# Kernel optimization log

Measured on AMD Instinct MI355X. Metric: run time of the kernel, lower is better.

## Reference

```python
import jax, jax.numpy as jnp
import numpy as np

N_NODES = 100000
N_EDGES = 800000
ANNOT = 92
HID = 64
N_STEPS = 8
N_IDX = 20000


def setup_inputs() -> dict:
    key = jax.random.key(0)
    ks = jax.random.split(key, 12)
    s = 1.0 / np.sqrt(HID)
    return {
        'x': jax.random.normal(ks[0], (N_NODES, ANNOT), dtype=jnp.float32),
        'edge_index': jax.random.randint(ks[1], (2, N_EDGES), 0, N_NODES, dtype=jnp.int64),
        'idx': jax.random.randint(ks[2], (N_IDX,), 0, N_NODES, dtype=jnp.int64),
        'W_red': jax.random.normal(ks[3], (ANNOT, HID), dtype=jnp.float32) / np.sqrt(ANNOT),
        'b_red': jnp.zeros((HID,), dtype=jnp.float32),
        'W_g': jax.random.normal(ks[4], (N_STEPS, HID, HID), dtype=jnp.float32) * s,
        'w_ih': jax.random.normal(ks[5], (3 * HID, HID), dtype=jnp.float32) * s,
        'w_hh': jax.random.normal(ks[6], (3 * HID, HID), dtype=jnp.float32) * s,
        'b_ih': jax.random.normal(ks[7], (3 * HID,), dtype=jnp.float32) * s,
        'b_hh': jax.random.normal(ks[8], (3 * HID,), dtype=jnp.float32) * s,
        'W_lin': jax.random.normal(ks[9], (HID, 1), dtype=jnp.float32) * s,
        'b_lin': jnp.zeros((1,), dtype=jnp.float32),
    }


def _gru_cell(a, h, w_ih, w_hh, b_ih, b_hh):
    # a: aggregated messages [N, H]; h: hidden state [N, H]
    gi = a @ w_ih.T + b_ih  # [N, 3H]
    gh = h @ w_hh.T + b_hh
    i_r, i_z, i_n = jnp.split(gi, 3, axis=-1)
    h_r, h_z, h_n = jnp.split(gh, 3, axis=-1)
    r = jax.nn.sigmoid(i_r + h_r)
    z = jax.nn.sigmoid(i_z + h_z)
    n = jnp.tanh(i_n + r * h_n)
    return (1.0 - z) * n + z * h


def reference(x, edge_index, idx, W_red, b_red, W_g, w_ih, w_hh, b_ih, b_hh, W_lin, b_lin):
    src, dst = edge_index[0], edge_index[1]
    h = x @ W_red + b_red  # [N, H]

    def step(h, Wt):
        m = h @ Wt                                  # [N, H] per-step transform
        msg = jnp.take(m, src, axis=0)              # gather along edges [E, H]
        aggr = jax.ops.segment_sum(msg, dst, num_segments=N_NODES)  # scatter-add
        h_new = _gru_cell(aggr, h, w_ih, w_hh, b_ih, b_hh)
        return h_new, None

    h, _ = jax.lax.scan(step, h, W_g)
    sel = jnp.take(h, idx, axis=0)                  # index_select [B, H]
    return jax.nn.sigmoid(sel @ W_lin + b_lin)      # [B, 1]
```

## Files before the change

kernel.cpp:

```cpp
#include <hip/hip_runtime.h>
#include <hip/hip_bf16.h>

#define NN 100000
#define HH 64
#define AN 92
#define NSTEP 8
#define NGRP 6250
#define NB 391
#define RB 768

typedef float f4v __attribute__((ext_vector_type(4)));
typedef short s8v __attribute__((ext_vector_type(8)));

__device__ __forceinline__ float sigf(float x) { return 1.0f / (1.0f + __expf(-x)); }
__device__ __forceinline__ float tanhfast(float x) { return 1.0f - 2.0f / (1.0f + __expf(2.0f * x)); }

__device__ __forceinline__ unsigned short tobf(float x) {
    __hip_bfloat16 b = __float2bfloat16(x);
    return __builtin_bit_cast(unsigned short, b);
}
__device__ __forceinline__ float frombf(unsigned short u) {
    return __int_as_float(((unsigned)u) << 16);
}

__device__ __forceinline__ int packpos(int k, int r) {
    int T = r >> 4, kh = k >> 5;
    int lane = ((k >> 3) & 3) * 16 + (r & 15);
    int j = k & 7;
    return ((T * 2 + kh) * 64 + lane) * 8 + j;
}

__global__ __launch_bounds__(256) void k_histwcp(const int* __restrict__ dst,
                                                 int* __restrict__ cur, int E, int HB,
                                                 const float* __restrict__ Wg,
                                                 const float* __restrict__ w_ih,
                                                 const float* __restrict__ w_hh,
                                                 unsigned short* __restrict__ Wcp,
                                                 unsigned short* __restrict__ Whp) {
    __shared__ float wl[192 * 65];
    if (blockIdx.x < HB) {
        int e = blockIdx.x * 256 + threadIdx.x;
        if (e < E) atomicAdd(cur + dst[e], 1);
        return;
    }
    int wb = blockIdx.x - HB;
    if (wb < 384) {
        for (int i = threadIdx.x; i < 192 * 64; i += 256) {
            int r = i >> 6, q = i & 63;
            wl[r * 65 + q] = w_ih[i];
        }
        __syncthreads();
        int gid = wb * 256 + threadIdx.x;
        int r = gid % 192;
        int k = (gid / 192) & 63;
        int t = gid / (192 * 64);
        const float* wg = Wg + t * 4096 + k * 64;
        float acc = 0.f;
#pragma unroll
        for (int q = 0; q < 64; ++q) acc = fmaf(wg[q], wl[r * 65 + q], acc);
        Wcp[t * 12288 + packpos(k, r)] = tobf(acc);
    } else {
        int gid = (wb - 384) * 256 + threadIdx.x;
        if (gid >= 192 * 64) return;
        int r = gid >> 6, k = gid & 63;
        Whp[packpos(k, r)] = tobf(w_hh[r * 64 + k]);
    }
}

__global__ __launch_bounds__(256) void k_scan1(const int* __restrict__ cur, int* __restrict__ bsum) {
    __shared__ int ws[4];
    int gid = blockIdx.x * 256 + threadIdx.x;
    int lane = threadIdx.x & 63, wave = threadIdx.x >> 6;
    int v = (gid < NN) ? cur[gid] : 0;
#pragma unroll
    for (int off = 32; off > 0; off >>= 1) v += __shfl_xor(v, off, 64);
    if (lane == 0) ws[wave] = v;
    __syncthreads();
    if (threadIdx.x == 0) bsum[blockIdx.x] = ws[0] + ws[1] + ws[2] + ws[3];
}

__global__ __launch_bounds__(256) void k_scan3(int* __restrict__ cur, const int* __restrict__ bsum) {
    __shared__ int ws[4];
    __shared__ int ws2[4];
    int tid = threadIdx.x;
    int lane = tid & 63, wave = tid >> 6;
    int s = 0;
    for (int i = tid; i < blockIdx.x; i += 256) s += bsum[i];
#pragma unroll
    for (int off = 32; off > 0; off >>= 1) s += __shfl_xor(s, off, 64);
    if (lane == 0) ws2[wave] = s;
    int gid = blockIdx.x * 256 + tid;
    int orig = (gid < NN) ? cur[gid] : 0;
    int v = orig;
#pragma unroll
    for (int off = 1; off < 64; off <<= 1) {
        int w = __shfl_up(v, off, 64);
        if (lane >= off) v += w;
    }
    if (lane == 63) ws[wave] = v;
    __syncthreads();
    int base = ws2[0] + ws2[1] + ws2[2] + ws2[3];
    int woff = 0;
    for (int w = 0; w < 4; ++w) woff += (w < wave) ? ws[w] : 0;
    if (gid < NN) cur[gid] = v - orig + woff + base;
}

__global__ __launch_bounds__(256) void k_plred(const int* __restrict__ src,
                                               const int* __restrict__ dst,
                                               int* __restrict__ cur,
                                               int* __restrict__ srt, int E,
                                               const float* __restrict__ x,
                                               const float* __restrict__ W,
                                               const float* __restrict__ b,
                                               float* __restrict__ h,
                                               unsigned short* __restrict__ hb) {
    __shared__ float xl[16][96];
    __shared__ float wl[96 * 64];
    int tid = threadIdx.x;
    if (blockIdx.x >= RB) {
        int e = (blockIdx.x - RB) * 256 + tid;
        if (e < E) {
            int pos = atomicAdd(cur + dst[e], 1);
            srt[pos] = src[e];
        }
        return;
    }
    for (int i = tid; i < AN * 64; i += 256) wl[i] = W[i];
    wl[AN * 64 + tid] = 0.f;
    if (tid < 64) xl[tid >> 2][AN + (tid & 3)] = 0.f;
    int lane = tid & 63, wave = tid >> 6;
    float bj = b[lane];

    for (int g = blockIdx.x; g < NGRP; g += RB) {
        int n0 = g * 16;
        __syncthreads();
        for (int i = tid; i < 16 * AN; i += 256)
            xl[i / AN][i % AN] = x[(size_t)n0 * AN + i];
        __syncthreads();
        float a[4];
#pragma unroll
        for (int u = 0; u < 4; ++u) a[u] = bj;
#pragma unroll
        for (int k4 = 0; k4 < 96; k4 += 4) {
            float4 xv[4];
#pragma unroll
            for (int u = 0; u < 4; ++u) xv[u] = *(const float4*)&xl[wave * 4 + u][k4];
#pragma unroll
            for (int kk = 0; kk < 4; ++kk) {
                float wv = wl[(k4 + kk) * 64 + lane];
                a[0] = fmaf(((const float*)&xv[0])[kk], wv, a[0]);
                a[1] = fmaf(((const float*)&xv[1])[kk], wv, a[1]);
                a[2] = fmaf(((const float*)&xv[2])[kk], wv, a[2]);
                a[3] = fmaf(((const float*)&xv[3])[kk], wv, a[3]);
            }
        }
#pragma unroll
        for (int u = 0; u < 4; ++u) {
            int n = n0 + wave * 4 + u;
            h[(size_t)n * HH + lane] = a[u];
            hb[(size_t)n * HH + lane] = tobf(a[u]);
        }
    }
}

__global__ __launch_bounds__(256) void k_aggr(const unsigned short* __restrict__ hb,
                                              const int* __restrict__ cur,
                                              const int* __restrict__ srt,
                                              unsigned short* __restrict__ Sb) {
    int gid = blockIdx.x * 256 + threadIdx.x;
    int wid = gid >> 6;
    int lane = threadIdx.x & 63;
    int half = lane >> 5;
    int ci = lane & 31;
    int n = wid * 2 + half;
    if (n >= NN) return;
    int st = (n == 0) ? 0 : cur[n - 1];
    int en = cur[n];
    float aa[8], bb[8];
#pragma unroll
    for (int i = 0; i < 8; ++i) { aa[i] = 0.f; bb[i] = 0.f; }
    for (int j = st; j < en; j += 8) {
        unsigned u[8];
#pragma unroll
        for (int i = 0; i < 8; ++i) {
            int jj = j + i;
            int sidx = srt[min(jj, en - 1)];
            unsigned uu = *(const unsigned*)(hb + (size_t)sidx * HH + ci * 2);
            u[i] = (jj < en) ? uu : 0u;
        }
#pragma unroll
        for (int i = 0; i < 8; ++i) {
            aa[i] += frombf((unsigned short)u[i]);
            bb[i] += frombf((unsigned short)(u[i] >> 16));
        }
    }
    float A = ((aa[0] + aa[1]) + (aa[2] + aa[3])) + ((aa[4] + aa[5]) + (aa[6] + aa[7]));
    float B = ((bb[0] + bb[1]) + (bb[2] + bb[3])) + ((bb[4] + bb[5]) + (bb[6] + bb[7]));
    unsigned o = (unsigned)tobf(A) | ((unsigned)tobf(B) << 16);
    *(unsigned*)(Sb + (size_t)n * HH + ci * 2) = o;
}

__device__ __forceinline__ s8v cvt8(const float* __restrict__ p) {
    s8v r;
#pragma unroll
    for (int i = 0; i < 8; ++i) r[i] = (short)tobf(p[i]);
    return r;
}

__global__ __launch_bounds__(256) void k_gru(const unsigned short* __restrict__ Sb,
                                             float* __restrict__ h,
                                             unsigned short* __restrict__ hb,
                                             const unsigned short* __restrict__ Wcp_t,
                                             const unsigned short* __restrict__ Whp,
                                             const float* __restrict__ b_ih,
                                             const float* __restrict__ b_hh) {
    const s8v* wiB = (const s8v*)Wcp_t;
    const s8v* whB = (const s8v*)Whp;

    int lane = threadIdx.x & 63;
    int wave = threadIdx.x >> 6;
    int quad = lane >> 4, nidx = lane & 15;
    int g = blockIdx.x * 4 + wave;
    if (g >= NGRP) return;

    float brz[4], bzz[4], bin[4], bhn[4];
#pragma unroll
    for (int t = 0; t < 4; ++t) {
        int c = t * 16 + nidx;
        brz[t] = b_ih[c] + b_hh[c];
        bzz[t] = b_ih[64 + c] + b_hh[64 + c];
        bin[t] = b_ih[128 + c];
        bhn[t] = b_hh[128 + c];
    }

    int n0 = g * 16;
    size_t rowoff = (size_t)(n0 + nidx) * HH + quad * 8;
    s8v aS0 = *(const s8v*)(Sb + rowoff);
    s8v aS1 = *(const s8v*)(Sb + rowoff + 32);
    s8v aH0 = cvt8(h + rowoff);
    s8v aH1 = cvt8(h + rowoff + 32);

#pragma unroll
    for (int t = 0; t < 4; ++t) {
        f4v aRZ0 = {brz[t], brz[t], brz[t], brz[t]};
        f4v aRZ1 = {bzz[t], bzz[t], bzz[t], bzz[t]};
        f4v aIN  = {bin[t], bin[t], bin[t], bin[t]};
        f4v aHN  = {bhn[t], bhn[t], bhn[t], bhn[t]};
        aRZ0 = __builtin_amdgcn_mfma_f32_16x16x32_bf16(aS0, wiB[(t * 2 + 0) * 64 + lane], aRZ0, 0, 0, 0);
        aRZ0 = __builtin_amdgcn_mfma_f32_16x16x32_bf16(aS1, wiB[(t * 2 + 1) * 64 + lane], aRZ0, 0, 0, 0);
        aRZ0 = __builtin_amdgcn_mfma_f32_16x16x32_bf16(aH0, whB[(t * 2 + 0) * 64 + lane], aRZ0, 0, 0, 0);
        aRZ0 = __builtin_amdgcn_mfma_f32_16x16x32_bf16(aH1, whB[(t * 2 + 1) * 64 + lane], aRZ0, 0, 0, 0);
        int tz = t + 4;
        aRZ1 = __builtin_amdgcn_mfma_f32_16x16x32_bf16(aS0, wiB[(tz * 2 + 0) * 64 + lane], aRZ1, 0, 0, 0);
        aRZ1 = __builtin_amdgcn_mfma_f32_16x16x32_bf16(aS1, wiB[(tz * 2 + 1) * 64 + lane], aRZ1, 0, 0, 0);
        aRZ1 = __builtin_amdgcn_mfma_f32_16x16x32_bf16(aH0, whB[(tz * 2 + 0) * 64 + lane], aRZ1, 0, 0, 0);
        aRZ1 = __builtin_amdgcn_mfma_f32_16x16x32_bf16(aH1, whB[(tz * 2 + 1) * 64 + lane], aRZ1, 0, 0, 0);
        int tn = t + 8;
        aIN = __builtin_amdgcn_mfma_f32_16x16x32_bf16(aS0, wiB[(tn * 2 + 0) * 64 + lane], aIN, 0, 0, 0);
        aIN = __builtin_amdgcn_mfma_f32_16x16x32_bf16(aS1, wiB[(tn * 2 + 1) * 64 + lane], aIN, 0, 0, 0);
        aHN = __builtin_amdgcn_mfma_f32_16x16x32_bf16(aH0, whB[(tn * 2 + 0) * 64 + lane], aHN, 0, 0, 0);
        aHN = __builtin_amdgcn_mfma_f32_16x16x32_bf16(aH1, whB[(tn * 2 + 1) * 64 + lane], aHN, 0, 0, 0);
        int c = t * 16 + nidx;
#pragma unroll
        for (int reg = 0; reg < 4; ++reg) {
            int node = n0 + quad * 4 + reg;
            float rv = sigf(aRZ0[reg]);
            float zv = sigf(aRZ1[reg]);
            float nv = tanhfast(fmaf(rv, aHN[reg], aIN[reg]));
            size_t off = (size_t)node * HH + c;
            float ho = h[off];
            float hnew = fmaf(zv, ho - nv, nv);
            h[off] = hnew;
            hb[off] = tobf(hnew);
        }
    }
}

__global__ __launch_bounds__(256) void k_readout(const float* __restrict__ h,
                                                 const int* __restrict__ idx,
                                                 const float* __restrict__ Wl,
                                                 const float* __restrict__ bl,
                                                 float* __restrict__ out, int B) {
    int gid = blockIdx.x * 256 + threadIdx.x;
    int i = gid >> 6, lane = gid & 63;
    if (i >= B) return;
    int n = idx[i];
    float v = h[(size_t)n * HH + lane] * Wl[lane];
#pragma unroll
    for (int off = 32; off > 0; off >>= 1) v += __shfl_xor(v, off, 64);
    if (lane == 0) out[i] = sigf(v + bl[0]);
}

extern "C" void kernel_launch(void* const* d_in, const int* in_sizes, int n_in,
                              void* d_out, int out_size, void* d_ws, size_t ws_size,
                              hipStream_t stream) {
    const float* x     = (const float*)d_in[0];
    const int*   ei    = (const int*)d_in[1];
    const int*   idx   = (const int*)d_in[2];
    const float* W_red = (const float*)d_in[3];
    const float* b_red = (const float*)d_in[4];
    const float* W_g   = (const float*)d_in[5];
    const float* w_ih  = (const float*)d_in[6];
    const float* w_hh  = (const float*)d_in[7];
    const float* b_ih  = (const float*)d_in[8];
    const float* b_hh  = (const float*)d_in[9];
    const float* W_lin = (const float*)d_in[10];
    const float* b_lin = (const float*)d_in[11];
    float* out = (float*)d_out;
    const int E = in_sizes[1] / 2;
    const int B = in_sizes[2];
    const int* src = ei;
    const int* dst = ei + E;
    const int PB = (E + 255) / 256;

    float*          h   = (float*)d_ws;
    unsigned short* hb  = (unsigned short*)(h + (size_t)NN * HH);
    unsigned short* Sb  = hb + (size_t)NN * HH;
    unsigned short* Wcp = Sb + (size_t)NN * HH;
    unsigned short* Whp = Wcp + (size_t)NSTEP * 12288;
    int*            cur = (int*)(Whp + 12288);
    int*            srt = cur + NN;
    int*            bsum = srt + E;

    hipMemsetAsync(cur, 0, NN * sizeof(int), stream);
    k_histwcp<<<PB + 384 + 48, 256, 0, stream>>>(dst, cur, E, PB,
                                                 W_g, w_ih, w_hh, Wcp, Whp);

    k_scan1<<<NB, 256, 0, stream>>>(cur, bsum);
    k_scan3<<<NB, 256, 0, stream>>>(cur, bsum);

    k_plred<<<RB + PB, 256, 0, stream>>>(src, dst, cur, srt, E,
                                         x, W_red, b_red, h, hb);

    for (int t = 0; t < NSTEP; ++t) {
        k_aggr<<<(NN / 2 * 64 + 255) / 256, 256, 0, stream>>>(hb, cur, srt, Sb);
        k_gru<<<1563, 256, 0, stream>>>(Sb, h, hb, Wcp + (size_t)t * 12288, Whp,
                                        b_ih, b_hh);
    }

    k_readout<<<(B * 64 + 255) / 256, 256, 0, stream>>>(h, idx, W_lin, b_lin, out, B);
}
```

Measured before the change: 580.8 us.

## Chunk bf16 hidden state by feature groups and aggregate one chunk per block

Stores the bf16 hidden state and the aggregate buffer as 8 column-chunks of 8 features each, laid out [chunk][node][8], so one gathered row is a single 16-byte load. Aggregation now runs one thread per node per chunk, with blockIdx selecting the chunk. The CSR offsets and the source indices for a block are staged in shared memory, with a global-memory fallback when a block's edge span exceeds the staging buffer. The intent is a gather table per chunk that is small enough to stay cache-resident and fewer, wider loads. The trade-off is that the sorted index list is read once per chunk and the GRU kernel now writes hb with scattered 2-byte stores.

```diff
diff --git a/kernel.cpp b/kernel.cpp
--- a/kernel.cpp
+++ b/kernel.cpp
@@ -8,6 +8,7 @@
 #define NGRP 6250
 #define NB 391
 #define RB 768
+#define SPMAX 4608
 
 typedef float f4v __attribute__((ext_vector_type(4)));
 typedef short s8v __attribute__((ext_vector_type(8)));
@@ -22,6 +23,7 @@
 __device__ __forceinline__ float frombf(unsigned short u) {
     return __int_as_float(((unsigned)u) << 16);
 }
+
 
 __device__ __forceinline__ int packpos(int k, int r) {
     int T = r >> 4, kh = k >> 5;
@@ -158,46 +160,75 @@
         for (int u = 0; u < 4; ++u) {
             int n = n0 + wave * 4 + u;
             h[(size_t)n * HH + lane] = a[u];
-            hb[(size_t)n * HH + lane] = tobf(a[u]);
-        }
-    }
-}
+            hb[((size_t)(lane >> 3) * NN + n) * 8 + (lane & 7)] = tobf(a[u]);
+        }
+    }
+}
+
+#define AGGR_BODY(GETSRC)                                                     \
+    for (int j = st; j < en; j += 4) {                                        \
+        unsigned u[4][4];                                                     \
+        _Pragma("unroll")                                                     \
+        for (int i = 0; i < 4; ++i) {                                         \
+            int jj = min(j + i, en - 1);                                      \
+            int sidx = GETSRC;                                                \
+            const uint4 uu = *(const uint4*)(tab + (size_t)sidx * 8);         \
+            unsigned m = (j + i < en) ? 0xffffffffu : 0u;                     \
+            u[i][0] = uu.x & m; u[i][1] = uu.y & m;                           \
+            u[i][2] = uu.z & m; u[i][3] = uu.w & m;                           \
+        }                                                                     \
+        _Pragma("unroll")                                                     \
+        for (int i = 0; i < 4; ++i) {                                         \
+            _Pragma("unroll")                                                 \
+            for (int k = 0; k < 4; ++k) {                                     \
+                unsigned w = u[i][k];                                         \
+                acc[2 * k]     += frombf((unsigned short)w);                  \
+                acc[2 * k + 1] += frombf((unsigned short)(w >> 16));          \
+            }                                                                 \
+        }                                                                     \
+    }
 
 __global__ __launch_bounds__(256) void k_aggr(const unsigned short* __restrict__ hb,
                                               const int* __restrict__ cur,
                                               const int* __restrict__ srt,
                                               unsigned short* __restrict__ Sb) {
-    int gid = blockIdx.x * 256 + threadIdx.x;
-    int wid = gid >> 6;
-    int lane = threadIdx.x & 63;
-    int half = lane >> 5;
-    int ci = lane & 31;
-    int n = wid * 2 + half;
+    __shared__ int s_srt[SPMAX];
+    __shared__ int s_cur[257];
+    const int cg = blockIdx.x & 7;
+    const int nb = blockIdx.x >> 3;
+    const int n0 = nb * 256;
+    const int tid = threadIdx.x;
+    for (int i = tid; i < 257; i += 256) {
+        int n = n0 + i - 1;
+        s_cur[i] = (n < 0) ? 0 : cur[min(n, NN - 1)];
+    }
+    __syncthreads();
+    const int base = s_cur[0];
+    const int span = s_cur[256] - base;
+    const int sp = min(span, SPMAX);
+    for (int i = tid; i < sp; i += 256) s_srt[i] = srt[base + i];
+    __syncthreads();
+    const int n = n0 + tid;
     if (n >= NN) return;
-    int st = (n == 0) ? 0 : cur[n - 1];
-    int en = cur[n];
-    float aa[8], bb[8];
-#pragma unroll
-    for (int i = 0; i < 8; ++i) { aa[i] = 0.f; bb[i] = 0.f; }
-    for (int j = st; j < en; j += 8) {
-        unsigned u[8];
-#pragma unroll
-        for (int i = 0; i < 8; ++i) {
-            int jj = j + i;
-            int sidx = srt[min(jj, en - 1)];
-            unsigned uu = *(const unsigned*)(hb + (size_t)sidx * HH + ci * 2);
-            u[i] = (jj < en) ? uu : 0u;
-        }
-#pragma unroll
-        for (int i = 0; i < 8; ++i) {
-            aa[i] += frombf((unsigned short)u[i]);
-            bb[i] += frombf((unsigned short)(u[i] >> 16));
-        }
-    }
-    float A = ((aa[0] + aa[1]) + (aa[2] + aa[3])) + ((aa[4] + aa[5]) + (aa[6] + aa[7]));
-    float B = ((bb[0] + bb[1]) + (bb[2] + bb[3])) + ((bb[4] + bb[5]) + (bb[6] + bb[7]));
-    unsigned o = (unsigned)tobf(A) | ((unsigned)tobf(B) << 16);
-    *(unsigned*)(Sb + (size_t)n * HH + ci * 2) = o;
+    const int st = s_cur[tid];
+    const int en = s_cur[tid + 1];
+    const unsigned short* tab = hb + (size_t)cg * (NN * 8);
+    float acc[8];
+#pragma unroll
+    for (int i = 0; i < 8; ++i) acc[i] = 0.f;
+
+    if (span <= SPMAX) {
+        AGGR_BODY(s_srt[jj - base])
+    } else {
+        AGGR_BODY(srt[jj])
+    }
+
+    unsigned o0 = (unsigned)tobf(acc[0]) | ((unsigned)tobf(acc[1]) << 16);
+    unsigned o1 = (unsigned)tobf(acc[2]) | ((unsigned)tobf(acc[3]) << 16);
+    unsigned o2 = (unsigned)tobf(acc[4]) | ((unsigned)tobf(acc[5]) << 16);
+    unsigned o3 = (unsigned)tobf(acc[6]) | ((unsigned)tobf(acc[7]) << 16);
+    uint4 ov; ov.x = o0; ov.y = o1; ov.z = o2; ov.w = o3;
+    *(uint4*)(Sb + ((size_t)cg * NN + n) * 8) = ov;
 }
 
 __device__ __forceinline__ s8v cvt8(const float* __restrict__ p) {
@@ -235,8 +266,9 @@
 
     int n0 = g * 16;
     size_t rowoff = (size_t)(n0 + nidx) * HH + quad * 8;
-    s8v aS0 = *(const s8v*)(Sb + rowoff);
-    s8v aS1 = *(const s8v*)(Sb + rowoff + 32);
+    size_t soff   = ((size_t)quad * NN + (n0 + nidx)) * 8;
+    s8v aS0 = *(const s8v*)(Sb + soff);
+    s8v aS1 = *(const s8v*)(Sb + soff + (size_t)4 * NN * 8);
     s8v aH0 = cvt8(h + rowoff);
     s8v aH1 = cvt8(h + rowoff + 32);
 
@@ -261,6 +293,8 @@
         aHN = __builtin_amdgcn_mfma_f32_16x16x32_bf16(aH0, whB[(tn * 2 + 0) * 64 + lane], aHN, 0, 0, 0);
         aHN = __builtin_amdgcn_mfma_f32_16x16x32_bf16(aH1, whB[(tn * 2 + 1) * 64 + lane], aHN, 0, 0, 0);
         int c = t * 16 + nidx;
+        int chunk = c >> 3;
+        int cc = c & 7;
 #pragma unroll
         for (int reg = 0; reg < 4; ++reg) {
             int node = n0 + quad * 4 + reg;
@@ -271,7 +305,7 @@
             float ho = h[off];
             float hnew = fmaf(zv, ho - nv, nv);
             h[off] = hnew;
-            hb[off] = tobf(hnew);
+            hb[((size_t)chunk * NN + node) * 8 + cc] = tobf(hnew);
         }
     }
 }
@@ -332,8 +366,9 @@
     k_plred<<<RB + PB, 256, 0, stream>>>(src, dst, cur, srt, E,
                                          x, W_red, b_red, h, hb);
 
+    const int AGB = ((NN + 255) / 256) * 8;
     for (int t = 0; t < NSTEP; ++t) {
-        k_aggr<<<(NN / 2 * 64 + 255) / 256, 256, 0, stream>>>(hb, cur, srt, Sb);
+        k_aggr<<<AGB, 256, 0, stream>>>(hb, cur, srt, Sb);
         k_gru<<<1563, 256, 0, stream>>>(Sb, h, hb, Wcp + (size_t)t * 12288, Whp,
                                         b_ih, b_hh);
     }
```

Result: slower. 699.1 us (+20.4%).

## Fuse edge aggregation and GRU update into one per-step kernel with ping-pong bf16 state

Applied to the files above, without the earlier changes.

Merges the gather/segment-sum kernel and the MFMA GRU kernel into a single per-step kernel. Each wave first aggregates its 16 nodes into a swizzled LDS tile, then feeds the tile straight into the MFMA GRU. This removes the global round trip of the aggregate buffer and halves the launches per step. To avoid read/write races on the bf16 hidden state across nodes, it double-buffers hb between steps. The trade-off is less parallelism during aggregation: one wave now handles 8 node pairs sequentially instead of one pair, which lowers memory-level parallelism for the latency-bound gathers.

```diff
diff --git a/kernel.cpp b/kernel.cpp
--- a/kernel.cpp
+++ b/kernel.cpp
@@ -163,65 +163,70 @@
     }
 }
 
-__global__ __launch_bounds__(256) void k_aggr(const unsigned short* __restrict__ hb,
+__device__ __forceinline__ s8v cvt8(const float* __restrict__ p) {
+    s8v r;
+#pragma unroll
+    for (int i = 0; i < 8; ++i) r[i] = (short)tobf(p[i]);
+    return r;
+}
+
+__global__ __launch_bounds__(256) void k_step(const unsigned short* __restrict__ hbo,
+                                              float* __restrict__ h,
+                                              unsigned short* __restrict__ hbn,
                                               const int* __restrict__ cur,
                                               const int* __restrict__ srt,
-                                              unsigned short* __restrict__ Sb) {
-    int gid = blockIdx.x * 256 + threadIdx.x;
-    int wid = gid >> 6;
+                                              const unsigned short* __restrict__ Wcp_t,
+                                              const unsigned short* __restrict__ Whp,
+                                              const float* __restrict__ b_ih,
+                                              const float* __restrict__ b_hh) {
+    __shared__ __align__(16) unsigned char sA[4][2048];
+
     int lane = threadIdx.x & 63;
-    int half = lane >> 5;
-    int ci = lane & 31;
-    int n = wid * 2 + half;
-    if (n >= NN) return;
-    int st = (n == 0) ? 0 : cur[n - 1];
-    int en = cur[n];
-    float aa[8], bb[8];
-#pragma unroll
-    for (int i = 0; i < 8; ++i) { aa[i] = 0.f; bb[i] = 0.f; }
-    for (int j = st; j < en; j += 8) {
-        unsigned u[8];
-#pragma unroll
-        for (int i = 0; i < 8; ++i) {
-            int jj = j + i;
-            int sidx = srt[min(jj, en - 1)];
-            unsigned uu = *(const unsigned*)(hb + (size_t)sidx * HH + ci * 2);
-            u[i] = (jj < en) ? uu : 0u;
-        }
-#pragma unroll
-        for (int i = 0; i < 8; ++i) {
-            aa[i] += frombf((unsigned short)u[i]);
-            bb[i] += frombf((unsigned short)(u[i] >> 16));
-        }
-    }
-    float A = ((aa[0] + aa[1]) + (aa[2] + aa[3])) + ((aa[4] + aa[5]) + (aa[6] + aa[7]));
-    float B = ((bb[0] + bb[1]) + (bb[2] + bb[3])) + ((bb[4] + bb[5]) + (bb[6] + bb[7]));
-    unsigned o = (unsigned)tobf(A) | ((unsigned)tobf(B) << 16);
-    *(unsigned*)(Sb + (size_t)n * HH + ci * 2) = o;
-}
-
-__device__ __forceinline__ s8v cvt8(const float* __restrict__ p) {
-    s8v r;
-#pragma unroll
-    for (int i = 0; i < 8; ++i) r[i] = (short)tobf(p[i]);
-    return r;
-}
-
-__global__ __launch_bounds__(256) void k_gru(const unsigned short* __restrict__ Sb,
-                                             float* __restrict__ h,
-                                             unsigned short* __restrict__ hb,
-                                             const unsigned short* __restrict__ Wcp_t,
-                                             const unsigned short* __restrict__ Whp,
-                                             const float* __restrict__ b_ih,
-                                             const float* __restrict__ b_hh) {
+    int wave = threadIdx.x >> 6;
+    int g = blockIdx.x * 4 + wave;
+    bool valid = g < NGRP;
+    int n0 = g * 16;
+
+    if (valid) {
+        int half = lane >> 5;
+        int ci = lane & 31;
+#pragma unroll 1
+        for (int p = 0; p < 8; ++p) {
+            int n = n0 + p * 2 + half;
+            int st = (n == 0) ? 0 : cur[n - 1];
+            int en = cur[n];
+            float aa[8], bb[8];
+#pragma unroll
+            for (int i = 0; i < 8; ++i) { aa[i] = 0.f; bb[i] = 0.f; }
+            for (int j = st; j < en; j += 8) {
+                unsigned u[8];
+#pragma unroll
+                for (int i = 0; i < 8; ++i) {
+                    int jj = j + i;
+                    int sidx = srt[min(jj, en - 1)];
+                    unsigned uu = *(const unsigned*)(hbo + (size_t)sidx * HH + ci * 2);
+                    u[i] = (jj < en) ? uu : 0u;
+                }
+#pragma unroll
+                for (int i = 0; i < 8; ++i) {
+                    aa[i] += frombf((unsigned short)u[i]);
+                    bb[i] += frombf((unsigned short)(u[i] >> 16));
+                }
+            }
+            float A = ((aa[0] + aa[1]) + (aa[2] + aa[3])) + ((aa[4] + aa[5]) + (aa[6] + aa[7]));
+            float B = ((bb[0] + bb[1]) + (bb[2] + bb[3])) + ((bb[4] + bb[5]) + (bb[6] + bb[7]));
+            unsigned o = (unsigned)tobf(A) | ((unsigned)tobf(B) << 16);
+            int row = p * 2 + half;
+            int cb = (row * 128 + ci * 4) ^ ((row & 7) << 4);
+            *(unsigned*)(&sA[wave][cb]) = o;
+        }
+    }
+    __syncthreads();
+    if (!valid) return;
+
     const s8v* wiB = (const s8v*)Wcp_t;
     const s8v* whB = (const s8v*)Whp;
-
-    int lane = threadIdx.x & 63;
-    int wave = threadIdx.x >> 6;
     int quad = lane >> 4, nidx = lane & 15;
-    int g = blockIdx.x * 4 + wave;
-    if (g >= NGRP) return;
 
     float brz[4], bzz[4], bin[4], bhn[4];
 #pragma unroll
@@ -233,10 +238,11 @@
         bhn[t] = b_hh[128 + c];
     }
 
-    int n0 = g * 16;
     size_t rowoff = (size_t)(n0 + nidx) * HH + quad * 8;
-    s8v aS0 = *(const s8v*)(Sb + rowoff);
-    s8v aS1 = *(const s8v*)(Sb + rowoff + 32);
+    int rb0 = (nidx * 128 + quad * 16) ^ ((nidx & 7) << 4);
+    int rb1 = (nidx * 128 + 64 + quad * 16) ^ ((nidx & 7) << 4);
+    s8v aS0 = *(const s8v*)(&sA[wave][rb0]);
+    s8v aS1 = *(const s8v*)(&sA[wave][rb1]);
     s8v aH0 = cvt8(h + rowoff);
     s8v aH1 = cvt8(h + rowoff + 32);
 
@@ -271,7 +277,7 @@
             float ho = h[off];
             float hnew = fmaf(zv, ho - nv, nv);
             h[off] = hnew;
-            hb[off] = tobf(hnew);
+            hbn[off] = tobf(hnew);
         }
     }
 }
@@ -314,13 +320,14 @@
     const int PB = (E + 255) / 256;
 
     float*          h   = (float*)d_ws;
-    unsigned short* hb  = (unsigned short*)(h + (size_t)NN * HH);
-    unsigned short* Sb  = hb + (size_t)NN * HH;
-    unsigned short* Wcp = Sb + (size_t)NN * HH;
+    unsigned short* hb0 = (unsigned short*)(h + (size_t)NN * HH);
+    unsigned short* hb1 = hb0 + (size_t)NN * HH;
+    unsigned short* Wcp = hb1 + (size_t)NN * HH;
     unsigned short* Whp = Wcp + (size_t)NSTEP * 12288;
     int*            cur = (int*)(Whp + 12288);
     int*            srt = cur + NN;
     int*            bsum = srt + E;
+    unsigned short* hbb[2] = {hb0, hb1};
 
     hipMemsetAsync(cur, 0, NN * sizeof(int), stream);
     k_histwcp<<<PB + 384 + 48, 256, 0, stream>>>(dst, cur, E, PB,
@@ -330,12 +337,13 @@
     k_scan3<<<NB, 256, 0, stream>>>(cur, bsum);
 
     k_plred<<<RB + PB, 256, 0, stream>>>(src, dst, cur, srt, E,
-                                         x, W_red, b_red, h, hb);
+                                         x, W_red, b_red, h, hb0);
 
     for (int t = 0; t < NSTEP; ++t) {
-        k_aggr<<<(NN / 2 * 64 + 255) / 256, 256, 0, stream>>>(hb, cur, srt, Sb);
-        k_gru<<<1563, 256, 0, stream>>>(Sb, h, hb, Wcp + (size_t)t * 12288, Whp,
-                                        b_ih, b_hh);
+        k_step<<<(NGRP + 3) / 4, 256, 0, stream>>>(hbb[t & 1], h, hbb[(t + 1) & 1],
+                                                   cur, srt,
+                                                   Wcp + (size_t)t * 12288, Whp,
+                                                   b_ih, b_hh);
     }
 
     k_readout<<<(B * 64 + 255) / 256, 256, 0, stream>>>(h, idx, W_lin, b_lin, out, B);
```

Result: slower. 715.9 us (+23.3%).
